# Performance work log

Measured on AMD Instinct MI355X. Metric: run time of the kernel, lower is better.

The kernel has to match this reference:

```python
import jax, jax.numpy as jnp
import numpy as np
import math

B, S, E, A = 8, 2048, 1024, 1024
NEG = -1e20

def setup_inputs() -> dict:
    key = jax.random.key(0)
    ks = jax.random.split(key, 6)
    scale = 1.0 / math.sqrt(E)
    return {
        "q": jax.random.normal(ks[0], (B, S, E), dtype=jnp.float32),
        "k": jax.random.normal(ks[1], (B, S, E), dtype=jnp.float32),
        "v": jax.random.normal(ks[2], (B, S, E), dtype=jnp.float32),
        "mask_pad": jnp.ones((B, S, S), dtype=jnp.int32),
        "Wq": jax.random.normal(ks[3], (E, A), dtype=jnp.float32) * scale,
        "Wk": jax.random.normal(ks[4], (E, A), dtype=jnp.float32) * scale,
        "Wv": jax.random.normal(ks[5], (E, A), dtype=jnp.float32) * scale,
    }

def reference(q, k, v, mask_pad, Wq, Wk, Wv):
    att_dim = Wq.shape[1]
    qp = jnp.einsum('bse,ea->bsa', q, Wq)
    kp = jnp.einsum('bse,ea->bsa', k, Wk)
    vp = jnp.einsum('bse,ea->bsa', v, Wv)
    # scores: [B, S, S]
    qk = jnp.einsum('bqa,bka->bqk', qp, kp) / jnp.sqrt(jnp.float32(att_dim))
    qk = jnp.where(mask_pad == 0, NEG, qk)
    # causal: torch.tril zeros out upper triangle, then zeros -> -1e20 (faithful quirk)
    seq = qk.shape[1]
    tril = jnp.tril(jnp.ones((seq, seq), dtype=bool))
    qk = jnp.where(tril[None, :, :], qk, 0.0)
    qk = jnp.where(qk == 0.0, NEG, qk)
    att_w = jax.nn.softmax(qk, axis=2)  # dropout p=0 -> identity
    return jnp.einsum('bqk,bka->bqa', att_w, vp)
```

## Files before the change

### kernel.cpp

```cpp
#include <hip/hip_runtime.h>
#include <math.h>

typedef __bf16 bf16x8 __attribute__((ext_vector_type(8)));
typedef float  f32x4  __attribute__((ext_vector_type(4)));
typedef unsigned short u16x8 __attribute__((ext_vector_type(8)));

#define NEGF (-1e20f)

__device__ __forceinline__ unsigned short f2bf(float f) {
  union { float f; unsigned u; } x; x.f = f;
  unsigned r = x.u + 0x7fffu + ((x.u >> 16) & 1u);
  return (unsigned short)(r >> 16);
}
__device__ __forceinline__ float bf2f(unsigned short h) {
  union { unsigned u; float f; } x; x.u = ((unsigned)h) << 16;
  return x.f;
}

__device__ __forceinline__ void gl16(const void* g, void* l) {
  __builtin_amdgcn_global_load_lds(
      (const __attribute__((address_space(1))) unsigned int*)g,
      (__attribute__((address_space(3))) unsigned int*)l, 16, 0, 0);
}
__device__ __forceinline__ unsigned lds_addr(const void* p) {
  return (unsigned)(unsigned long long)(const __attribute__((address_space(3))) char*)p;
}

#define DSR(dst, off) asm volatile("ds_read_b128 %0, %1" : "=v"(dst) : "v"(off))
#define LGKM0 asm volatile("s_waitcnt lgkmcnt(0)" ::: "memory")
#define VMC0  asm volatile("s_waitcnt vmcnt(0)" ::: "memory")
#define SBAR  __builtin_amdgcn_s_barrier()
#define SCH0  __builtin_amdgcn_sched_barrier(0)

__global__ __launch_bounds__(256) void k_cvt3(
    const float* __restrict__ q, const float* __restrict__ k, const float* __restrict__ v,
    unsigned short* __restrict__ qo, unsigned short* __restrict__ ko, unsigned short* __restrict__ vo) {
  const float* in = (blockIdx.y == 0) ? q : (blockIdx.y == 1) ? k : v;
  unsigned short* out = (blockIdx.y == 0) ? qo : (blockIdx.y == 1) ? ko : vo;
  size_t i = ((size_t)blockIdx.x * 256 + threadIdx.x) * 8;
  const float4* p = (const float4*)(in + i);
  float4 a = p[0], b = p[1];
  u16x8 o;
  o[0] = f2bf(a.x); o[1] = f2bf(a.y); o[2] = f2bf(a.z); o[3] = f2bf(a.w);
  o[4] = f2bf(b.x); o[5] = f2bf(b.y); o[6] = f2bf(b.z); o[7] = f2bf(b.w);
  *(u16x8*)(out + i) = o;
}

__global__ __launch_bounds__(256) void k_cvt_w(const float* __restrict__ W,
                                               unsigned short* __restrict__ WT) {
  __shared__ float t[32][33];
  const int tid = threadIdx.x;
  const int tx = tid & 31, ty = tid >> 5;
  const int e0 = blockIdx.y * 32, a0 = blockIdx.x * 32;
#pragma unroll
  for (int i = 0; i < 4; i++) {
    int el = ty + i * 8;
    t[el][tx] = W[(size_t)(e0 + el) * 1024 + a0 + tx];
  }
  __syncthreads();
#pragma unroll
  for (int i = 0; i < 4; i++) {
    int al = ty + i * 8;
    WT[(size_t)(a0 + al) * 1024 + e0 + tx] = f2bf(t[tx][al]);
  }
}

__global__ __launch_bounds__(256) void k_maskbits(const int* __restrict__ mask,
                                                  unsigned short* __restrict__ bits) {
  size_t t = (size_t)blockIdx.x * 256 + threadIdx.x;
  const int4* p = (const int4*)(mask + t * 16);
  int4 a = p[0], b = p[1], c = p[2], d = p[3];
  unsigned m = 0;
  m |= (a.x != 0) ? 1u : 0u;      m |= (a.y != 0) ? 2u : 0u;
  m |= (a.z != 0) ? 4u : 0u;      m |= (a.w != 0) ? 8u : 0u;
  m |= (b.x != 0) ? 16u : 0u;     m |= (b.y != 0) ? 32u : 0u;
  m |= (b.z != 0) ? 64u : 0u;     m |= (b.w != 0) ? 128u : 0u;
  m |= (c.x != 0) ? 256u : 0u;    m |= (c.y != 0) ? 512u : 0u;
  m |= (c.z != 0) ? 1024u : 0u;   m |= (c.w != 0) ? 2048u : 0u;
  m |= (d.x != 0) ? 4096u : 0u;   m |= (d.y != 0) ? 8192u : 0u;
  m |= (d.z != 0) ? 16384u : 0u;  m |= (d.w != 0) ? 32768u : 0u;
  bits[t] = (unsigned short)m;
}

__device__ __forceinline__ void tile128_gemm(
    const unsigned short* __restrict__ A, int lda,
    const unsigned short* __restrict__ Bt, int ldb,
    int brow, int bcol, int NT,
    unsigned short* AsBase, unsigned short* BsBase,
    int wr, int wc, int fr, int fq,
    f32x4 (&acc)[4][4])
{
  const int tid = threadIdx.x, wid = tid >> 6, l = tid & 63;
  const int sr = l >> 3;
  const int sc = ((l & 7) ^ sr) * 8;

  const unsigned short* ga = A + (size_t)(brow + wid * 32 + sr) * lda + sc;
  const unsigned short* gb = Bt + (size_t)(bcol + wid * 32 + sr) * ldb + sc;

  unsigned aA[4], aB[4];
#pragma unroll
  for (int m = 0; m < 4; m++) aA[m] = lds_addr(AsBase) + (unsigned)((wr * 64 + m * 16 + fr) * 128);
#pragma unroll
  for (int n = 0; n < 4; n++) aB[n] = lds_addr(BsBase) + (unsigned)((wc * 64 + n * 16 + fr) * 128);
  const unsigned ck0 = (unsigned)((fq ^ (fr & 7)) * 16);
  const unsigned ck1 = (unsigned)(((4 + fq) ^ (fr & 7)) * 16);

  auto stage = [&](int buf, int k0) {
    unsigned short* la = AsBase + buf * (128 * 64);
    unsigned short* lb = BsBase + buf * (128 * 64);
#pragma unroll
    for (int i = 0; i < 4; i++) {
      gl16(ga + (size_t)(8 * i) * lda + k0, la + (wid * 32 + 8 * i) * 64);
      gl16(gb + (size_t)(8 * i) * ldb + k0, lb + (wid * 32 + 8 * i) * 64);
    }
  };

  stage(0, 0);
  VMC0; SBAR;

  for (int t = 0; t < NT; ++t) {
    if (t + 1 < NT) stage((t + 1) & 1, (t + 1) << 6);
    const unsigned bo = (unsigned)((t & 1) * (128 * 64 * 2));
    u16x8 ar[4], br[4];
#pragma unroll
    for (int m = 0; m < 4; m++) DSR(ar[m], aA[m] + bo + ck0);
#pragma unroll
    for (int n = 0; n < 4; n++) DSR(br[n], aB[n] + bo + ck0);
    LGKM0; SCH0;
    __builtin_amdgcn_s_setprio(1);
#pragma unroll
    for (int m = 0; m < 4; m++)
#pragma unroll
      for (int n = 0; n < 4; n++)
        acc[m][n] = __builtin_amdgcn_mfma_f32_16x16x32_bf16(
            __builtin_bit_cast(bf16x8, ar[m]), __builtin_bit_cast(bf16x8, br[n]), acc[m][n], 0, 0, 0);
    __builtin_amdgcn_s_setprio(0);
    u16x8 ar2[4], br2[4];
#pragma unroll
    for (int m = 0; m < 4; m++) DSR(ar2[m], aA[m] + bo + ck1);
#pragma unroll
    for (int n = 0; n < 4; n++) DSR(br2[n], aB[n] + bo + ck1);
    LGKM0; SCH0;
    __builtin_amdgcn_s_setprio(1);
#pragma unroll
    for (int m = 0; m < 4; m++)
#pragma unroll
      for (int n = 0; n < 4; n++)
        acc[m][n] = __builtin_amdgcn_mfma_f32_16x16x32_bf16(
            __builtin_bit_cast(bf16x8, ar2[m]), __builtin_bit_cast(bf16x8, br2[n]), acc[m][n], 0, 0, 0);
    __builtin_amdgcn_s_setprio(0);
    SCH0;
    VMC0;
    SBAR;
  }
}

__global__ __launch_bounds__(512, 2) void k_proj256(
    const unsigned short* __restrict__ A, int lda,
    const unsigned short* __restrict__ Bt, int ldb,
    unsigned short* __restrict__ C, int ldc, int K, float scale)
{
  const int nwg = gridDim.x * gridDim.y;
  int lin = blockIdx.y * gridDim.x + blockIdx.x;
  int swz = (lin & 7) * (nwg >> 3) + (lin >> 3);
  const int bx = swz % gridDim.x, by = swz / gridDim.x;
  const int brow = by * 256, bcol = bx * 256;

  __shared__ unsigned short As[2][256 * 64];
  __shared__ unsigned short Bs[2][256 * 64];

  const int tid = threadIdx.x, w = tid >> 6, l = tid & 63;
  const int wr = w >> 2, wc = w & 3;
  const int fr = l & 15, fq = l >> 4;
  const int sr = l >> 3;
  const int sc = ((l & 7) ^ sr) * 8;

  const unsigned short* ga = A + (size_t)(brow + w * 32 + sr) * lda + sc;
  const unsigned short* gb = Bt + (size_t)(bcol + w * 32 + sr) * ldb + sc;

  f32x4 acc[8][4] = {};

  unsigned aA[8], aB[4];
#pragma unroll
  for (int m = 0; m < 8; m++) aA[m] = lds_addr(&As[0][0]) + (unsigned)((wr * 128 + m * 16 + fr) * 128);
#pragma unroll
  for (int n = 0; n < 4; n++) aB[n] = lds_addr(&Bs[0][0]) + (unsigned)((wc * 64 + n * 16 + fr) * 128);
  const unsigned ck0 = (unsigned)((fq ^ (fr & 7)) * 16);
  const unsigned ck1 = (unsigned)(((4 + fq) ^ (fr & 7)) * 16);

  auto stage = [&](int buf, int k0) {
#pragma unroll
    for (int i = 0; i < 4; i++) {
      gl16(ga + (size_t)(8 * i) * lda + k0, &As[buf][(w * 32 + 8 * i) * 64]);
      gl16(gb + (size_t)(8 * i) * ldb + k0, &Bs[buf][(w * 32 + 8 * i) * 64]);
    }
  };

  const int NT = K >> 6;
  stage(0, 0);
  VMC0; SBAR;
  for (int t = 0; t < NT; ++t) {
    if (t + 1 < NT) stage((t + 1) & 1, (t + 1) << 6);
    const unsigned bo = (unsigned)((t & 1) * (256 * 64 * 2));
    u16x8 ar[8], br[4];
#pragma unroll
    for (int m = 0; m < 8; m++) DSR(ar[m], aA[m] + bo + ck0);
#pragma unroll
    for (int n = 0; n < 4; n++) DSR(br[n], aB[n] + bo + ck0);
    LGKM0; SCH0;
    __builtin_amdgcn_s_setprio(1);
#pragma unroll
    for (int m = 0; m < 8; m++)
#pragma unroll
      for (int n = 0; n < 4; n++)
        acc[m][n] = __builtin_amdgcn_mfma_f32_16x16x32_bf16(
            __builtin_bit_cast(bf16x8, ar[m]), __builtin_bit_cast(bf16x8, br[n]), acc[m][n], 0, 0, 0);
    __builtin_amdgcn_s_setprio(0);
    u16x8 ar2[8], br2[4];
#pragma unroll
    for (int m = 0; m < 8; m++) DSR(ar2[m], aA[m] + bo + ck1);
#pragma unroll
    for (int n = 0; n < 4; n++) DSR(br2[n], aB[n] + bo + ck1);
    LGKM0; SCH0;
    __builtin_amdgcn_s_setprio(1);
#pragma unroll
    for (int m = 0; m < 8; m++)
#pragma unroll
      for (int n = 0; n < 4; n++)
        acc[m][n] = __builtin_amdgcn_mfma_f32_16x16x32_bf16(
            __builtin_bit_cast(bf16x8, ar2[m]), __builtin_bit_cast(bf16x8, br2[n]), acc[m][n], 0, 0, 0);
    __builtin_amdgcn_s_setprio(0);
    SCH0;
    VMC0; SBAR;
  }

#pragma unroll
  for (int m = 0; m < 8; m++)
#pragma unroll
    for (int n = 0; n < 4; n++)
#pragma unroll
      for (int r = 0; r < 4; r++) {
        int rg = brow + wr * 128 + m * 16 + fq * 4 + r;
        int cg = bcol + wc * 64 + n * 16 + fr;
        C[(size_t)rg * ldc + cg] = f2bf(acc[m][n][r] * scale);
      }
}

__global__ __launch_bounds__(256, 2) void k_scores(
    const unsigned short* __restrict__ QP,
    const unsigned short* __restrict__ KP,
    unsigned short* __restrict__ S,
    const unsigned short* __restrict__ maskbits)
{
  int bid0 = blockIdx.x;
  int bid = (bid0 & 7) * 136 + (bid0 >> 3);
  const int b = bid / 136;
  int t0 = bid - b * 136;
  int by = (int)((sqrtf((float)(8 * t0 + 1)) - 1.0f) * 0.5f);
  if ((by + 1) * (by + 2) / 2 <= t0) by++;
  else if (by * (by + 1) / 2 > t0) by--;
  const int bx = t0 - (by * (by + 1)) / 2;
  const int brow = by * 128, bcol = bx * 128;

  const unsigned short* A  = QP + (size_t)b * (2048 * 1024);
  const unsigned short* Bt = KP + (size_t)b * (2048 * 1024);

  __shared__ unsigned short As[2][128 * 64];
  __shared__ unsigned short Bs[2][128 * 64];

  const int tid = threadIdx.x, wid = tid >> 6, lane = tid & 63;
  const int wr = wid >> 1, wc = wid & 1;
  const int fr = lane & 15, fq = lane >> 4;

  const unsigned short* bits = maskbits + (size_t)b * 2048 * 128;
  unsigned mbits[2] = {0u, 0u};
#pragma unroll
  for (int m = 0; m < 4; m++)
#pragma unroll
    for (int r = 0; r < 4; r++) {
      int qq = brow + wr * 64 + m * 16 + fq * 4 + r;
      unsigned long long mw =
          *(const unsigned long long*)(bits + (size_t)qq * 128 + ((bcol + wc * 64) >> 4));
#pragma unroll
      for (int n = 0; n < 4; n++) {
        int jj = (m << 4) | (n << 2) | r;
        unsigned bit = (unsigned)((mw >> (n * 16 + fr)) & 1ull);
        mbits[jj >> 5] |= bit << (jj & 31);
      }
    }
  asm volatile("" ::: "memory");

  f32x4 acc[4][4] = {};
  tile128_gemm(A, 1024, Bt, 1024, brow, bcol, 16, &As[0][0], &Bs[0][0],
               wr, wc, fr, fq, acc);

  unsigned short* Cb = S + (size_t)b * 2048 * 2048;
#pragma unroll
  for (int m = 0; m < 4; m++)
#pragma unroll
    for (int n = 0; n < 4; n++)
#pragma unroll
      for (int r = 0; r < 4; r++) {
        int jj = (m << 4) | (n << 2) | r;
        int qq = brow + wr * 64 + m * 16 + fq * 4 + r;
        int kk = bcol + wc * 64 + n * 16 + fr;
        float s = acc[m][n][r];
        if (!((mbits[jj >> 5] >> (jj & 31)) & 1u)) s = NEGF;
        if (kk > qq) s = NEGF;
        else if (s == 0.0f) s = NEGF;
        Cb[(size_t)qq * 2048 + kk] = f2bf(s);
      }
}

__global__ __launch_bounds__(256, 2) void k_pv(
    const unsigned short* __restrict__ P,
    const unsigned short* __restrict__ VpT,
    float* __restrict__ Out)
{
  const int b = blockIdx.z;
  const int by = (int)(gridDim.y - 1 - blockIdx.y);
  const int bx = blockIdx.x;
  const int brow = by * 128, bcol = bx * 128;

  const unsigned short* A  = P + (size_t)b * 2048 * 2048;
  const unsigned short* Bt = VpT + (size_t)b * 2048;

  __shared__ unsigned short As[2][128 * 64];
  __shared__ unsigned short Bs[2][128 * 64];

  const int tid = threadIdx.x, wid = tid >> 6, lane = tid & 63;
  const int wr = wid >> 1, wc = wid & 1;
  const int fr = lane & 15, fq = lane >> 4;

  f32x4 acc[4][4] = {};
  const int NT = (brow + 128) >> 6;
  tile128_gemm(A, 2048, Bt, 16384, brow, bcol, NT, &As[0][0], &Bs[0][0],
               wr, wc, fr, fq, acc);

  float* C = Out + (size_t)b * 2048 * 1024;
#pragma unroll
  for (int m = 0; m < 4; m++)
#pragma unroll
    for (int n = 0; n < 4; n++)
#pragma unroll
      for (int r = 0; r < 4; r++) {
        int rg = brow + wr * 64 + m * 16 + fq * 4 + r;
        int cg = bcol + wc * 64 + n * 16 + fr;
        C[(size_t)rg * 1024 + cg] = acc[m][n][r];
      }
}

__global__ __launch_bounds__(256) void k_softmax_bf(unsigned short* __restrict__ S) {
  const int row = blockIdx.x;
  const int qq = row & 2047;
  const int L = ((qq >> 7) + 1) << 7;
  const int tid = threadIdx.x;
  unsigned short* p = S + (size_t)row * 2048;
  float val[8];
  float mx = -3.0e38f;
  int cnt = 0;
  for (int i = tid; i * 4 < L; i += 256) {
    ushort4 u = *(const ushort4*)(p + i * 4);
    float a = bf2f(u.x), bb = bf2f(u.y), c = bf2f(u.z), d = bf2f(u.w);
    val[cnt] = a; val[cnt + 1] = bb; val[cnt + 2] = c; val[cnt + 3] = d;
    mx = fmaxf(fmaxf(fmaxf(mx, a), bb), fmaxf(c, d));
    cnt += 4;
  }
#pragma unroll
  for (int o = 32; o; o >>= 1) mx = fmaxf(mx, __shfl_xor(mx, o));
  __shared__ float sred[8];
  if ((tid & 63) == 0) sred[tid >> 6] = mx;
  __syncthreads();
  mx = fmaxf(fmaxf(sred[0], sred[1]), fmaxf(sred[2], sred[3]));
  float sum = 0.f;
  for (int j = 0; j < cnt; j++) { val[j] = __expf(val[j] - mx); sum += val[j]; }
#pragma unroll
  for (int o = 32; o; o >>= 1) sum += __shfl_xor(sum, o);
  if ((tid & 63) == 0) sred[4 + (tid >> 6)] = sum;
  __syncthreads();
  sum = (sred[4] + sred[5]) + (sred[6] + sred[7]);
  const float inv = 1.0f / sum;
  int j = 0;
  for (int i = tid; i * 4 < L; i += 256) {
    ushort4 o;
    o.x = f2bf(val[j] * inv);     o.y = f2bf(val[j + 1] * inv);
    o.z = f2bf(val[j + 2] * inv); o.w = f2bf(val[j + 3] * inv);
    *(ushort4*)(p + i * 4) = o;
    j += 4;
  }
}

extern "C" void kernel_launch(void* const* d_in, const int* in_sizes, int n_in,
                              void* d_out, int out_size, void* d_ws, size_t ws_size,
                              hipStream_t stream) {
  const float* q   = (const float*)d_in[0];
  const float* k   = (const float*)d_in[1];
  const float* v   = (const float*)d_in[2];
  const int*   msk = (const int*)d_in[3];
  const float* Wq  = (const float*)d_in[4];
  const float* Wk  = (const float*)d_in[5];
  const float* Wv  = (const float*)d_in[6];
  float* out = (float*)d_out;

  char* ws = (char*)d_ws;
  unsigned short* WqT = (unsigned short*)(ws + 0);
  unsigned short* WkT = (unsigned short*)(ws + 2097152);
  unsigned short* WvT = (unsigned short*)(ws + 4194304);
  unsigned short* qp  = (unsigned short*)(ws + 6291456);
  unsigned short* kp  = (unsigned short*)(ws + 39845888);
  unsigned short* vpT = (unsigned short*)(ws + 73400320);
  unsigned short* qbf = (unsigned short*)(ws + 106954752);
  unsigned short* kbf = (unsigned short*)(ws + 140509184);
  unsigned short* vbf = (unsigned short*)(ws + 174063616);
  unsigned short* P = (unsigned short*)(ws + 106954752);
  unsigned short* mbitsbuf = (unsigned short*)(ws + 207618048);

  dim3 blk(256), blk5(512);
  k_cvt3<<<dim3(8192, 3), blk, 0, stream>>>(q, k, v, qbf, kbf, vbf);
  k_cvt_w<<<dim3(32, 32), blk, 0, stream>>>(Wq, WqT);
  k_cvt_w<<<dim3(32, 32), blk, 0, stream>>>(Wk, WkT);
  k_cvt_w<<<dim3(32, 32), blk, 0, stream>>>(Wv, WvT);
  k_maskbits<<<dim3(8192), blk, 0, stream>>>(msk, mbitsbuf);

  k_proj256<<<dim3(4, 64), blk5, 0, stream>>>(qbf, 1024, WqT, 1024, qp, 1024, 1024, 0.03125f);
  k_proj256<<<dim3(4, 64), blk5, 0, stream>>>(kbf, 1024, WkT, 1024, kp, 1024, 1024, 1.0f);
  k_proj256<<<dim3(64, 4), blk5, 0, stream>>>(WvT, 1024, vbf, 1024, vpT, 16384, 1024, 1.0f);

  k_scores<<<dim3(1088), blk, 0, stream>>>(qp, kp, P, mbitsbuf);

  k_softmax_bf<<<dim3(16384), blk, 0, stream>>>(P);

  k_pv<<<dim3(8, 16, 8), blk, 0, stream>>>(P, vpT, out);
  (void)in_sizes; (void)n_in; (void)out_size; (void)ws_size;
}
```

Baseline: 365.8 us.

## Fuse fp32-to-bf16 activation conversion into projection GEMM loads

The projection GEMM now reads fp32 q/k/v directly, converts them to bf16 in registers and writes them into swizzled LDS, which removes the separate conversion kernel and its bf16 round trip through global memory. The three weight-transpose launches are merged into a single 3D-grid launch, and the mask-packing kernel now processes four chunks per thread with a quarter of the blocks. In exchange the GEMM loads twice as many bytes per element for one operand through ordinary register loads instead of direct-to-LDS loads, adding VGPR pressure and a VALU conversion step inside the main loop.

New measurement: 378.5 us. +3.5%, slower.

```diff
diff --git a/kernel.cpp b/kernel.cpp
--- a/kernel.cpp
+++ b/kernel.cpp
@@ -11,6 +11,10 @@
   union { float f; unsigned u; } x; x.f = f;
   unsigned r = x.u + 0x7fffu + ((x.u >> 16) & 1u);
   return (unsigned short)(r >> 16);
+}
+__device__ __forceinline__ unsigned short f2bfh(float f) {
+  __bf16 h = (__bf16)f;
+  return __builtin_bit_cast(unsigned short, h);
 }
 __device__ __forceinline__ float bf2f(unsigned short h) {
   union { unsigned u; float f; } x; x.u = ((unsigned)h) << 16;
@@ -32,22 +36,11 @@
 #define SBAR  __builtin_amdgcn_s_barrier()
 #define SCH0  __builtin_amdgcn_sched_barrier(0)
 
-__global__ __launch_bounds__(256) void k_cvt3(
-    const float* __restrict__ q, const float* __restrict__ k, const float* __restrict__ v,
-    unsigned short* __restrict__ qo, unsigned short* __restrict__ ko, unsigned short* __restrict__ vo) {
-  const float* in = (blockIdx.y == 0) ? q : (blockIdx.y == 1) ? k : v;
-  unsigned short* out = (blockIdx.y == 0) ? qo : (blockIdx.y == 1) ? ko : vo;
-  size_t i = ((size_t)blockIdx.x * 256 + threadIdx.x) * 8;
-  const float4* p = (const float4*)(in + i);
-  float4 a = p[0], b = p[1];
-  u16x8 o;
-  o[0] = f2bf(a.x); o[1] = f2bf(a.y); o[2] = f2bf(a.z); o[3] = f2bf(a.w);
-  o[4] = f2bf(b.x); o[5] = f2bf(b.y); o[6] = f2bf(b.z); o[7] = f2bf(b.w);
-  *(u16x8*)(out + i) = o;
-}
-
-__global__ __launch_bounds__(256) void k_cvt_w(const float* __restrict__ W,
-                                               unsigned short* __restrict__ WT) {
+__global__ __launch_bounds__(256) void k_cvt_w3(
+    const float* __restrict__ Wq, const float* __restrict__ Wk, const float* __restrict__ Wv,
+    unsigned short* __restrict__ Tq, unsigned short* __restrict__ Tk, unsigned short* __restrict__ Tv) {
+  const float* W = (blockIdx.z == 0) ? Wq : (blockIdx.z == 1) ? Wk : Wv;
+  unsigned short* WT = (blockIdx.z == 0) ? Tq : (blockIdx.z == 1) ? Tk : Tv;
   __shared__ float t[32][33];
   const int tid = threadIdx.x;
   const int tx = tid & 31, ty = tid >> 5;
@@ -67,19 +60,148 @@
 
 __global__ __launch_bounds__(256) void k_maskbits(const int* __restrict__ mask,
                                                   unsigned short* __restrict__ bits) {
-  size_t t = (size_t)blockIdx.x * 256 + threadIdx.x;
-  const int4* p = (const int4*)(mask + t * 16);
-  int4 a = p[0], b = p[1], c = p[2], d = p[3];
-  unsigned m = 0;
-  m |= (a.x != 0) ? 1u : 0u;      m |= (a.y != 0) ? 2u : 0u;
-  m |= (a.z != 0) ? 4u : 0u;      m |= (a.w != 0) ? 8u : 0u;
-  m |= (b.x != 0) ? 16u : 0u;     m |= (b.y != 0) ? 32u : 0u;
-  m |= (b.z != 0) ? 64u : 0u;     m |= (b.w != 0) ? 128u : 0u;
-  m |= (c.x != 0) ? 256u : 0u;    m |= (c.y != 0) ? 512u : 0u;
-  m |= (c.z != 0) ? 1024u : 0u;   m |= (c.w != 0) ? 2048u : 0u;
-  m |= (d.x != 0) ? 4096u : 0u;   m |= (d.y != 0) ? 8192u : 0u;
-  m |= (d.z != 0) ? 16384u : 0u;  m |= (d.w != 0) ? 32768u : 0u;
-  bits[t] = (unsigned short)m;
+#pragma unroll
+  for (int it = 0; it < 4; it++) {
+    size_t t = (size_t)it * 524288 + (size_t)blockIdx.x * 256 + threadIdx.x;
+    const int4* p = (const int4*)(mask + t * 16);
+    int4 a = p[0], b = p[1], c = p[2], d = p[3];
+    unsigned m = 0;
+    m |= (a.x != 0) ? 1u : 0u;      m |= (a.y != 0) ? 2u : 0u;
+    m |= (a.z != 0) ? 4u : 0u;      m |= (a.w != 0) ? 8u : 0u;
+    m |= (b.x != 0) ? 16u : 0u;     m |= (b.y != 0) ? 32u : 0u;
+    m |= (b.z != 0) ? 64u : 0u;     m |= (b.w != 0) ? 128u : 0u;
+    m |= (c.x != 0) ? 256u : 0u;    m |= (c.y != 0) ? 512u : 0u;
+    m |= (c.z != 0) ? 1024u : 0u;   m |= (c.w != 0) ? 2048u : 0u;
+    m |= (d.x != 0) ? 4096u : 0u;   m |= (d.y != 0) ? 8192u : 0u;
+    m |= (d.z != 0) ? 16384u : 0u;  m |= (d.w != 0) ? 32768u : 0u;
+    bits[t] = (unsigned short)m;
+  }
+}
+
+template<int FSIDE>
+__global__ __launch_bounds__(512, 2) void k_proj256(
+    const float* __restrict__ F, int ldf,
+    const unsigned short* __restrict__ H, int ldh,
+    unsigned short* __restrict__ C, int ldc, float scale)
+{
+  const int nwg = gridDim.x * gridDim.y;
+  int lin = blockIdx.y * gridDim.x + blockIdx.x;
+  int swz = (lin & 7) * (nwg >> 3) + (lin >> 3);
+  const int bx = swz % gridDim.x, by = swz / gridDim.x;
+  const int brow = by * 256, bcol = bx * 256;
+
+  __shared__ unsigned short As[2][256 * 64];
+  __shared__ unsigned short Bs[2][256 * 64];
+
+  const int tid = threadIdx.x, w = tid >> 6, l = tid & 63;
+  const int wr = w >> 2, wc = w & 3;
+  const int fr = l & 15, fq = l >> 4;
+
+  const int sr4 = tid >> 3;
+  const int scn = tid & 7;
+  const int hr = l >> 3;
+  const int hc = ((l & 7) ^ hr) * 8;
+
+  const int fbase = (FSIDE == 0) ? brow : bcol;
+  const int hbase = (FSIDE == 0) ? bcol : brow;
+  const float* gF = F + (size_t)(fbase + sr4 * 4) * ldf + scn * 8;
+  const unsigned short* gH = H + (size_t)(hbase + w * 32 + hr) * ldh + hc;
+
+  unsigned short* Fl = (FSIDE == 0) ? &As[0][0] : &Bs[0][0];
+  unsigned short* Hl = (FSIDE == 0) ? &Bs[0][0] : &As[0][0];
+
+  f32x4 acc[8][4] = {};
+
+  unsigned aA[8], aB[4];
+#pragma unroll
+  for (int m = 0; m < 8; m++) aA[m] = lds_addr(&As[0][0]) + (unsigned)((wr * 128 + m * 16 + fr) * 128);
+#pragma unroll
+  for (int n = 0; n < 4; n++) aB[n] = lds_addr(&Bs[0][0]) + (unsigned)((wc * 64 + n * 16 + fr) * 128);
+  const unsigned ck0 = (unsigned)((fq ^ (fr & 7)) * 16);
+  const unsigned ck1 = (unsigned)(((4 + fq) ^ (fr & 7)) * 16);
+
+  float4 fa[8];
+  auto loadF = [&](int k0) {
+#pragma unroll
+    for (int i = 0; i < 4; i++) {
+      const float* p = gF + (size_t)i * ldf + k0;
+      fa[2 * i]     = *(const float4*)p;
+      fa[2 * i + 1] = *(const float4*)(p + 4);
+    }
+  };
+  auto writeF = [&](int buf) {
+    unsigned short* lb = Fl + buf * (256 * 64);
+#pragma unroll
+    for (int i = 0; i < 4; i++) {
+      int row = sr4 * 4 + i;
+      u16x8 o;
+      o[0] = f2bfh(fa[2 * i].x);     o[1] = f2bfh(fa[2 * i].y);
+      o[2] = f2bfh(fa[2 * i].z);     o[3] = f2bfh(fa[2 * i].w);
+      o[4] = f2bfh(fa[2 * i + 1].x); o[5] = f2bfh(fa[2 * i + 1].y);
+      o[6] = f2bfh(fa[2 * i + 1].z); o[7] = f2bfh(fa[2 * i + 1].w);
+      *(u16x8*)&lb[row * 64 + ((scn ^ (row & 7)) * 8)] = o;
+    }
+  };
+  auto stageH = [&](int buf, int k0) {
+    unsigned short* lb = Hl + buf * (256 * 64);
+#pragma unroll
+    for (int i = 0; i < 4; i++)
+      gl16(gH + (size_t)(8 * i) * ldh + k0, lb + (w * 32 + 8 * i) * 64);
+  };
+
+  const int NT = 16;
+  loadF(0); stageH(0, 0);
+  VMC0;
+  writeF(0);
+  LGKM0; SBAR;
+
+  for (int t = 0; t < NT; ++t) {
+    if (t + 1 < NT) { loadF((t + 1) << 6); stageH((t + 1) & 1, (t + 1) << 6); SCH0; }
+    const unsigned bo = (unsigned)((t & 1) * (256 * 64 * 2));
+    u16x8 ar[8], br[4];
+#pragma unroll
+    for (int m = 0; m < 8; m++) DSR(ar[m], aA[m] + bo + ck0);
+#pragma unroll
+    for (int n = 0; n < 4; n++) DSR(br[n], aB[n] + bo + ck0);
+    LGKM0; SCH0;
+    __builtin_amdgcn_s_setprio(1);
+#pragma unroll
+    for (int m = 0; m < 8; m++)
+#pragma unroll
+      for (int n = 0; n < 4; n++)
+        acc[m][n] = __builtin_amdgcn_mfma_f32_16x16x32_bf16(
+            __builtin_bit_cast(bf16x8, ar[m]), __builtin_bit_cast(bf16x8, br[n]), acc[m][n], 0, 0, 0);
+    __builtin_amdgcn_s_setprio(0);
+    u16x8 ar2[8], br2[4];
+#pragma unroll
+    for (int m = 0; m < 8; m++) DSR(ar2[m], aA[m] + bo + ck1);
+#pragma unroll
+    for (int n = 0; n < 4; n++) DSR(br2[n], aB[n] + bo + ck1);
+    LGKM0; SCH0;
+    __builtin_amdgcn_s_setprio(1);
+#pragma unroll
+    for (int m = 0; m < 8; m++)
+#pragma unroll
+      for (int n = 0; n < 4; n++)
+        acc[m][n] = __builtin_amdgcn_mfma_f32_16x16x32_bf16(
+            __builtin_bit_cast(bf16x8, ar2[m]), __builtin_bit_cast(bf16x8, br2[n]), acc[m][n], 0, 0, 0);
+    __builtin_amdgcn_s_setprio(0);
+    SCH0;
+    VMC0;
+    if (t + 1 < NT) writeF((t + 1) & 1);
+    LGKM0; SBAR;
+  }
+
+#pragma unroll
+  for (int m = 0; m < 8; m++)
+#pragma unroll
+    for (int n = 0; n < 4; n++)
+#pragma unroll
+      for (int r = 0; r < 4; r++) {
+        int rg = brow + wr * 128 + m * 16 + fq * 4 + r;
+        int cg = bcol + wc * 64 + n * 16 + fr;
+        C[(size_t)rg * ldc + cg] = f2bf(acc[m][n][r] * scale);
+      }
 }
 
 __device__ __forceinline__ void tile128_gemm(
@@ -153,97 +275,6 @@
     VMC0;
     SBAR;
   }
-}
-
-__global__ __launch_bounds__(512, 2) void k_proj256(
-    const unsigned short* __restrict__ A, int lda,
-    const unsigned short* __restrict__ Bt, int ldb,
-    unsigned short* __restrict__ C, int ldc, int K, float scale)
-{
-  const int nwg = gridDim.x * gridDim.y;
-  int lin = blockIdx.y * gridDim.x + blockIdx.x;
-  int swz = (lin & 7) * (nwg >> 3) + (lin >> 3);
-  const int bx = swz % gridDim.x, by = swz / gridDim.x;
-  const int brow = by * 256, bcol = bx * 256;
-
-  __shared__ unsigned short As[2][256 * 64];
-  __shared__ unsigned short Bs[2][256 * 64];
-
-  const int tid = threadIdx.x, w = tid >> 6, l = tid & 63;
-  const int wr = w >> 2, wc = w & 3;
-  const int fr = l & 15, fq = l >> 4;
-  const int sr = l >> 3;
-  const int sc = ((l & 7) ^ sr) * 8;
-
-  const unsigned short* ga = A + (size_t)(brow + w * 32 + sr) * lda + sc;
-  const unsigned short* gb = Bt + (size_t)(bcol + w * 32 + sr) * ldb + sc;
-
-  f32x4 acc[8][4] = {};
-
-  unsigned aA[8], aB[4];
-#pragma unroll
-  for (int m = 0; m < 8; m++) aA[m] = lds_addr(&As[0][0]) + (unsigned)((wr * 128 + m * 16 + fr) * 128);
-#pragma unroll
-  for (int n = 0; n < 4; n++) aB[n] = lds_addr(&Bs[0][0]) + (unsigned)((wc * 64 + n * 16 + fr) * 128);
-  const unsigned ck0 = (unsigned)((fq ^ (fr & 7)) * 16);
-  const unsigned ck1 = (unsigned)(((4 + fq) ^ (fr & 7)) * 16);
-
-  auto stage = [&](int buf, int k0) {
-#pragma unroll
-    for (int i = 0; i < 4; i++) {
-      gl16(ga + (size_t)(8 * i) * lda + k0, &As[buf][(w * 32 + 8 * i) * 64]);
-      gl16(gb + (size_t)(8 * i) * ldb + k0, &Bs[buf][(w * 32 + 8 * i) * 64]);
-    }
-  };
-
-  const int NT = K >> 6;
-  stage(0, 0);
-  VMC0; SBAR;
-  for (int t = 0; t < NT; ++t) {
-    if (t + 1 < NT) stage((t + 1) & 1, (t + 1) << 6);
-    const unsigned bo = (unsigned)((t & 1) * (256 * 64 * 2));
-    u16x8 ar[8], br[4];
-#pragma unroll
-    for (int m = 0; m < 8; m++) DSR(ar[m], aA[m] + bo + ck0);
-#pragma unroll
-    for (int n = 0; n < 4; n++) DSR(br[n], aB[n] + bo + ck0);
-    LGKM0; SCH0;
-    __builtin_amdgcn_s_setprio(1);
-#pragma unroll
-    for (int m = 0; m < 8; m++)
-#pragma unroll
-      for (int n = 0; n < 4; n++)
-        acc[m][n] = __builtin_amdgcn_mfma_f32_16x16x32_bf16(
-            __builtin_bit_cast(bf16x8, ar[m]), __builtin_bit_cast(bf16x8, br[n]), acc[m][n], 0, 0, 0);
-    __builtin_amdgcn_s_setprio(0);
-    u16x8 ar2[8], br2[4];
-#pragma unroll
-    for (int m = 0; m < 8; m++) DSR(ar2[m], aA[m] + bo + ck1);
-#pragma unroll
-    for (int n = 0; n < 4; n++) DSR(br2[n], aB[n] + bo + ck1);
-    LGKM0; SCH0;
-    __builtin_amdgcn_s_setprio(1);
-#pragma unroll
-    for (int m = 0; m < 8; m++)
-#pragma unroll
-      for (int n = 0; n < 4; n++)
-        acc[m][n] = __builtin_amdgcn_mfma_f32_16x16x32_bf16(
-            __builtin_bit_cast(bf16x8, ar2[m]), __builtin_bit_cast(bf16x8, br2[n]), acc[m][n], 0, 0, 0);
-    __builtin_amdgcn_s_setprio(0);
-    SCH0;
-    VMC0; SBAR;
-  }
-
-#pragma unroll
-  for (int m = 0; m < 8; m++)
-#pragma unroll
-    for (int n = 0; n < 4; n++)
-#pragma unroll
-      for (int r = 0; r < 4; r++) {
-        int rg = brow + wr * 128 + m * 16 + fq * 4 + r;
-        int cg = bcol + wc * 64 + n * 16 + fr;
-        C[(size_t)rg * ldc + cg] = f2bf(acc[m][n][r] * scale);
-      }
 }
 
 __global__ __launch_bounds__(256, 2) void k_scores(
@@ -409,22 +440,16 @@
   unsigned short* qp  = (unsigned short*)(ws + 6291456);
   unsigned short* kp  = (unsigned short*)(ws + 39845888);
   unsigned short* vpT = (unsigned short*)(ws + 73400320);
-  unsigned short* qbf = (unsigned short*)(ws + 106954752);
-  unsigned short* kbf = (unsigned short*)(ws + 140509184);
-  unsigned short* vbf = (unsigned short*)(ws + 174063616);
-  unsigned short* P = (unsigned short*)(ws + 106954752);
+  unsigned short* P   = (unsigned short*)(ws + 106954752);
   unsigned short* mbitsbuf = (unsigned short*)(ws + 207618048);
 
   dim3 blk(256), blk5(512);
-  k_cvt3<<<dim3(8192, 3), blk, 0, stream>>>(q, k, v, qbf, kbf, vbf);
-  k_cvt_w<<<dim3(32, 32), blk, 0, stream>>>(Wq, WqT);
-  k_cvt_w<<<dim3(32, 32), blk, 0, stream>>>(Wk, WkT);
-  k_cvt_w<<<dim3(32, 32), blk, 0, stream>>>(Wv, WvT);
-  k_maskbits<<<dim3(8192), blk, 0, stream>>>(msk, mbitsbuf);
-
-  k_proj256<<<dim3(4, 64), blk5, 0, stream>>>(qbf, 1024, WqT, 1024, qp, 1024, 1024, 0.03125f);
-  k_proj256<<<dim3(4, 64), blk5, 0, stream>>>(kbf, 1024, WkT, 1024, kp, 1024, 1024, 1.0f);
-  k_proj256<<<dim3(64, 4), blk5, 0, stream>>>(WvT, 1024, vbf, 1024, vpT, 16384, 1024, 1.0f);
+  k_cvt_w3<<<dim3(32, 32, 3), blk, 0, stream>>>(Wq, Wk, Wv, WqT, WkT, WvT);
+  k_maskbits<<<dim3(2048), blk, 0, stream>>>(msk, mbitsbuf);
+
+  k_proj256<0><<<dim3(4, 64), blk5, 0, stream>>>(q, 1024, WqT, 1024, qp, 1024, 0.03125f);
+  k_proj256<0><<<dim3(4, 64), blk5, 0, stream>>>(k, 1024, WkT, 1024, kp, 1024, 1.0f);
+  k_proj256<1><<<dim3(64, 4), blk5, 0, stream>>>(v, 1024, WvT, 1024, vpT, 16384, 1.0f);
 
   k_scores<<<dim3(1088), blk, 0, stream>>>(qp, kp, P, mbitsbuf);
 
```

## Enlarge scores and PV GEMM tiles to 256x256 with shared core

Applied to the files above, without the earlier changes.

Replaces the 128x128 tiled scores and PV kernels with 256x256 tiles on 512-thread blocks, reusing a common gemm256_core that is also used by the projection kernel. Causal block granularity becomes 256, so the softmax row length and skipped tiles are adjusted to match. Larger tiles raise data reuse per loaded byte but compute more masked work along the diagonal and reduce the number of blocks, which may hurt load balance. Also merges the three weight conversions into one launch and widens the input conversion to 16 elements per thread using native bf16 casts.

Result: slower. 433.8 us (+18.6%).

```diff
diff --git a/kernel.cpp b/kernel.cpp
--- a/kernel.cpp
+++ b/kernel.cpp
@@ -11,6 +11,10 @@
   union { float f; unsigned u; } x; x.f = f;
   unsigned r = x.u + 0x7fffu + ((x.u >> 16) & 1u);
   return (unsigned short)(r >> 16);
+}
+__device__ __forceinline__ unsigned short f2bfh(float f) {
+  __bf16 h = (__bf16)f;
+  return __builtin_bit_cast(unsigned short, h);
 }
 __device__ __forceinline__ float bf2f(unsigned short h) {
   union { unsigned u; float f; } x; x.u = ((unsigned)h) << 16;
@@ -37,17 +41,23 @@
     unsigned short* __restrict__ qo, unsigned short* __restrict__ ko, unsigned short* __restrict__ vo) {
   const float* in = (blockIdx.y == 0) ? q : (blockIdx.y == 1) ? k : v;
   unsigned short* out = (blockIdx.y == 0) ? qo : (blockIdx.y == 1) ? ko : vo;
-  size_t i = ((size_t)blockIdx.x * 256 + threadIdx.x) * 8;
+  size_t i = ((size_t)blockIdx.x * 256 + threadIdx.x) * 16;
   const float4* p = (const float4*)(in + i);
-  float4 a = p[0], b = p[1];
-  u16x8 o;
-  o[0] = f2bf(a.x); o[1] = f2bf(a.y); o[2] = f2bf(a.z); o[3] = f2bf(a.w);
-  o[4] = f2bf(b.x); o[5] = f2bf(b.y); o[6] = f2bf(b.z); o[7] = f2bf(b.w);
-  *(u16x8*)(out + i) = o;
-}
-
-__global__ __launch_bounds__(256) void k_cvt_w(const float* __restrict__ W,
-                                               unsigned short* __restrict__ WT) {
+  float4 a = p[0], b = p[1], c = p[2], d = p[3];
+  u16x8 o0, o1;
+  o0[0] = f2bfh(a.x); o0[1] = f2bfh(a.y); o0[2] = f2bfh(a.z); o0[3] = f2bfh(a.w);
+  o0[4] = f2bfh(b.x); o0[5] = f2bfh(b.y); o0[6] = f2bfh(b.z); o0[7] = f2bfh(b.w);
+  o1[0] = f2bfh(c.x); o1[1] = f2bfh(c.y); o1[2] = f2bfh(c.z); o1[3] = f2bfh(c.w);
+  o1[4] = f2bfh(d.x); o1[5] = f2bfh(d.y); o1[6] = f2bfh(d.z); o1[7] = f2bfh(d.w);
+  *(u16x8*)(out + i) = o0;
+  *(u16x8*)(out + i + 8) = o1;
+}
+
+__global__ __launch_bounds__(256) void k_cvt_w3(
+    const float* __restrict__ Wq, const float* __restrict__ Wk, const float* __restrict__ Wv,
+    unsigned short* __restrict__ Tq, unsigned short* __restrict__ Tk, unsigned short* __restrict__ Tv) {
+  const float* W = (blockIdx.z == 0) ? Wq : (blockIdx.z == 1) ? Wk : Wv;
+  unsigned short* WT = (blockIdx.z == 0) ? Tq : (blockIdx.z == 1) ? Tk : Tv;
   __shared__ float t[32][33];
   const int tid = threadIdx.x;
   const int tx = tid & 31, ty = tid >> 5;
@@ -82,83 +92,80 @@
   bits[t] = (unsigned short)m;
 }
 
-__device__ __forceinline__ void tile128_gemm(
+__device__ __forceinline__ void gemm256_core(
     const unsigned short* __restrict__ A, int lda,
     const unsigned short* __restrict__ Bt, int ldb,
     int brow, int bcol, int NT,
-    unsigned short* AsBase, unsigned short* BsBase,
-    int wr, int wc, int fr, int fq,
-    f32x4 (&acc)[4][4])
+    unsigned short* As0, unsigned short* Bs0,
+    f32x4 (&acc)[8][4])
 {
-  const int tid = threadIdx.x, wid = tid >> 6, l = tid & 63;
-  const int sr = l >> 3;
-  const int sc = ((l & 7) ^ sr) * 8;
-
-  const unsigned short* ga = A + (size_t)(brow + wid * 32 + sr) * lda + sc;
-  const unsigned short* gb = Bt + (size_t)(bcol + wid * 32 + sr) * ldb + sc;
-
-  unsigned aA[4], aB[4];
-#pragma unroll
-  for (int m = 0; m < 4; m++) aA[m] = lds_addr(AsBase) + (unsigned)((wr * 64 + m * 16 + fr) * 128);
-#pragma unroll
-  for (int n = 0; n < 4; n++) aB[n] = lds_addr(BsBase) + (unsigned)((wc * 64 + n * 16 + fr) * 128);
+  const int tid = threadIdx.x, w = tid >> 6, l = tid & 63;
+  const int wr = w >> 2, wc = w & 3;
+  const int fr = l & 15, fq = l >> 4;
+  const int hr = l >> 3;
+  const int hc = ((l & 7) ^ hr) * 8;
+
+  const unsigned short* ga = A + (size_t)(brow + w * 32 + hr) * lda + hc;
+  const unsigned short* gb = Bt + (size_t)(bcol + w * 32 + hr) * ldb + hc;
+
+  unsigned aA[8], aB[4];
+#pragma unroll
+  for (int m = 0; m < 8; m++) aA[m] = lds_addr(As0) + (unsigned)((wr * 128 + m * 16 + fr) * 128);
+#pragma unroll
+  for (int n = 0; n < 4; n++) aB[n] = lds_addr(Bs0) + (unsigned)((wc * 64 + n * 16 + fr) * 128);
   const unsigned ck0 = (unsigned)((fq ^ (fr & 7)) * 16);
   const unsigned ck1 = (unsigned)(((4 + fq) ^ (fr & 7)) * 16);
 
   auto stage = [&](int buf, int k0) {
-    unsigned short* la = AsBase + buf * (128 * 64);
-    unsigned short* lb = BsBase + buf * (128 * 64);
 #pragma unroll
     for (int i = 0; i < 4; i++) {
-      gl16(ga + (size_t)(8 * i) * lda + k0, la + (wid * 32 + 8 * i) * 64);
-      gl16(gb + (size_t)(8 * i) * ldb + k0, lb + (wid * 32 + 8 * i) * 64);
+      gl16(ga + (size_t)(8 * i) * lda + k0, As0 + buf * (256 * 64) + (w * 32 + 8 * i) * 64);
+      gl16(gb + (size_t)(8 * i) * ldb + k0, Bs0 + buf * (256 * 64) + (w * 32 + 8 * i) * 64);
     }
   };
 
   stage(0, 0);
   VMC0; SBAR;
-
   for (int t = 0; t < NT; ++t) {
     if (t + 1 < NT) stage((t + 1) & 1, (t + 1) << 6);
-    const unsigned bo = (unsigned)((t & 1) * (128 * 64 * 2));
-    u16x8 ar[4], br[4];
-#pragma unroll
-    for (int m = 0; m < 4; m++) DSR(ar[m], aA[m] + bo + ck0);
+    const unsigned bo = (unsigned)((t & 1) * (256 * 64 * 2));
+    u16x8 ar[8], br[4];
+#pragma unroll
+    for (int m = 0; m < 8; m++) DSR(ar[m], aA[m] + bo + ck0);
 #pragma unroll
     for (int n = 0; n < 4; n++) DSR(br[n], aB[n] + bo + ck0);
     LGKM0; SCH0;
     __builtin_amdgcn_s_setprio(1);
 #pragma unroll
-    for (int m = 0; m < 4; m++)
+    for (int m = 0; m < 8; m++)
 #pragma unroll
       for (int n = 0; n < 4; n++)
         acc[m][n] = __builtin_amdgcn_mfma_f32_16x16x32_bf16(
             __builtin_bit_cast(bf16x8, ar[m]), __builtin_bit_cast(bf16x8, br[n]), acc[m][n], 0, 0, 0);
     __builtin_amdgcn_s_setprio(0);
-    u16x8 ar2[4], br2[4];
-#pragma unroll
-    for (int m = 0; m < 4; m++) DSR(ar2[m], aA[m] + bo + ck1);
+    u16x8 ar2[8], br2[4];
+#pragma unroll
+    for (int m = 0; m < 8; m++) DSR(ar2[m], aA[m] + bo + ck1);
 #pragma unroll
     for (int n = 0; n < 4; n++) DSR(br2[n], aB[n] + bo + ck1);
     LGKM0; SCH0;
     __builtin_amdgcn_s_setprio(1);
 #pragma unroll
-    for (int m = 0; m < 4; m++)
+    for (int m = 0; m < 8; m++)
 #pragma unroll
       for (int n = 0; n < 4; n++)
         acc[m][n] = __builtin_amdgcn_mfma_f32_16x16x32_bf16(
             __builtin_bit_cast(bf16x8, ar2[m]), __builtin_bit_cast(bf16x8, br2[n]), acc[m][n], 0, 0, 0);
     __builtin_amdgcn_s_setprio(0);
     SCH0;
-    VMC0;
-    SBAR;
+    VMC0; SBAR;
   }
 }
 
 __global__ __launch_bounds__(512, 2) void k_proj256(
     const unsigned short* __restrict__ A, int lda,
     const unsigned short* __restrict__ Bt, int ldb,
-    unsigned short* __restrict__ C, int ldc, int K, float scale)
+    unsigned short* __restrict__ C, int ldc, float scale)
 {
   const int nwg = gridDim.x * gridDim.y;
   int lin = blockIdx.y * gridDim.x + blockIdx.x;
@@ -168,71 +175,12 @@
 
   __shared__ unsigned short As[2][256 * 64];
   __shared__ unsigned short Bs[2][256 * 64];
-
   const int tid = threadIdx.x, w = tid >> 6, l = tid & 63;
   const int wr = w >> 2, wc = w & 3;
   const int fr = l & 15, fq = l >> 4;
-  const int sr = l >> 3;
-  const int sc = ((l & 7) ^ sr) * 8;
-
-  const unsigned short* ga = A + (size_t)(brow + w * 32 + sr) * lda + sc;
-  const unsigned short* gb = Bt + (size_t)(bcol + w * 32 + sr) * ldb + sc;
 
   f32x4 acc[8][4] = {};
-
-  unsigned aA[8], aB[4];
-#pragma unroll
-  for (int m = 0; m < 8; m++) aA[m] = lds_addr(&As[0][0]) + (unsigned)((wr * 128 + m * 16 + fr) * 128);
-#pragma unroll
-  for (int n = 0; n < 4; n++) aB[n] = lds_addr(&Bs[0][0]) + (unsigned)((wc * 64 + n * 16 + fr) * 128);
-  const unsigned ck0 = (unsigned)((fq ^ (fr & 7)) * 16);
-  const unsigned ck1 = (unsigned)(((4 + fq) ^ (fr & 7)) * 16);
-
-  auto stage = [&](int buf, int k0) {
-#pragma unroll
-    for (int i = 0; i < 4; i++) {
-      gl16(ga + (size_t)(8 * i) * lda + k0, &As[buf][(w * 32 + 8 * i) * 64]);
-      gl16(gb + (size_t)(8 * i) * ldb + k0, &Bs[buf][(w * 32 + 8 * i) * 64]);
-    }
-  };
-
-  const int NT = K >> 6;
-  stage(0, 0);
-  VMC0; SBAR;
-  for (int t = 0; t < NT; ++t) {
-    if (t + 1 < NT) stage((t + 1) & 1, (t + 1) << 6);
-    const unsigned bo = (unsigned)((t & 1) * (256 * 64 * 2));
-    u16x8 ar[8], br[4];
-#pragma unroll
-    for (int m = 0; m < 8; m++) DSR(ar[m], aA[m] + bo + ck0);
-#pragma unroll
-    for (int n = 0; n < 4; n++) DSR(br[n], aB[n] + bo + ck0);
-    LGKM0; SCH0;
-    __builtin_amdgcn_s_setprio(1);
-#pragma unroll
-    for (int m = 0; m < 8; m++)
-#pragma unroll
-      for (int n = 0; n < 4; n++)
-        acc[m][n] = __builtin_amdgcn_mfma_f32_16x16x32_bf16(
-            __builtin_bit_cast(bf16x8, ar[m]), __builtin_bit_cast(bf16x8, br[n]), acc[m][n], 0, 0, 0);
-    __builtin_amdgcn_s_setprio(0);
-    u16x8 ar2[8], br2[4];
-#pragma unroll
-    for (int m = 0; m < 8; m++) DSR(ar2[m], aA[m] + bo + ck1);
-#pragma unroll
-    for (int n = 0; n < 4; n++) DSR(br2[n], aB[n] + bo + ck1);
-    LGKM0; SCH0;
-    __builtin_amdgcn_s_setprio(1);
-#pragma unroll
-    for (int m = 0; m < 8; m++)
-#pragma unroll
-      for (int n = 0; n < 4; n++)
-        acc[m][n] = __builtin_amdgcn_mfma_f32_16x16x32_bf16(
-            __builtin_bit_cast(bf16x8, ar2[m]), __builtin_bit_cast(bf16x8, br2[n]), acc[m][n], 0, 0, 0);
-    __builtin_amdgcn_s_setprio(0);
-    SCH0;
-    VMC0; SBAR;
-  }
+  gemm256_core(A, lda, Bt, ldb, brow, bcol, 16, &As[0][0], &Bs[0][0], acc);
 
 #pragma unroll
   for (int m = 0; m < 8; m++)
@@ -246,39 +194,37 @@
       }
 }
 
-__global__ __launch_bounds__(256, 2) void k_scores(
+__global__ __launch_bounds__(512, 2) void k_scores256(
     const unsigned short* __restrict__ QP,
     const unsigned short* __restrict__ KP,
     unsigned short* __restrict__ S,
     const unsigned short* __restrict__ maskbits)
 {
-  int bid0 = blockIdx.x;
-  int bid = (bid0 & 7) * 136 + (bid0 >> 3);
-  const int b = bid / 136;
-  int t0 = bid - b * 136;
+  int bid = ((int)blockIdx.x & 7) * 36 + ((int)blockIdx.x >> 3);
+  const int b = bid / 36;
+  int t0 = bid - b * 36;
   int by = (int)((sqrtf((float)(8 * t0 + 1)) - 1.0f) * 0.5f);
   if ((by + 1) * (by + 2) / 2 <= t0) by++;
   else if (by * (by + 1) / 2 > t0) by--;
   const int bx = t0 - (by * (by + 1)) / 2;
-  const int brow = by * 128, bcol = bx * 128;
+  const int brow = by * 256, bcol = bx * 256;
 
   const unsigned short* A  = QP + (size_t)b * (2048 * 1024);
   const unsigned short* Bt = KP + (size_t)b * (2048 * 1024);
 
-  __shared__ unsigned short As[2][128 * 64];
-  __shared__ unsigned short Bs[2][128 * 64];
-
-  const int tid = threadIdx.x, wid = tid >> 6, lane = tid & 63;
-  const int wr = wid >> 1, wc = wid & 1;
-  const int fr = lane & 15, fq = lane >> 4;
+  __shared__ unsigned short As[2][256 * 64];
+  __shared__ unsigned short Bs[2][256 * 64];
+  const int tid = threadIdx.x, w = tid >> 6, l = tid & 63;
+  const int wr = w >> 2, wc = w & 3;
+  const int fr = l & 15, fq = l >> 4;
 
   const unsigned short* bits = maskbits + (size_t)b * 2048 * 128;
-  unsigned mbits[2] = {0u, 0u};
-#pragma unroll
-  for (int m = 0; m < 4; m++)
+  unsigned mbits[4] = {0u, 0u, 0u, 0u};
+#pragma unroll
+  for (int m = 0; m < 8; m++)
 #pragma unroll
     for (int r = 0; r < 4; r++) {
-      int qq = brow + wr * 64 + m * 16 + fq * 4 + r;
+      int qq = brow + wr * 128 + m * 16 + fq * 4 + r;
       unsigned long long mw =
           *(const unsigned long long*)(bits + (size_t)qq * 128 + ((bcol + wc * 64) >> 4));
 #pragma unroll
@@ -290,19 +236,18 @@
     }
   asm volatile("" ::: "memory");
 
-  f32x4 acc[4][4] = {};
-  tile128_gemm(A, 1024, Bt, 1024, brow, bcol, 16, &As[0][0], &Bs[0][0],
-               wr, wc, fr, fq, acc);
+  f32x4 acc[8][4] = {};
+  gemm256_core(A, 1024, Bt, 1024, brow, bcol, 16, &As[0][0], &Bs[0][0], acc);
 
   unsigned short* Cb = S + (size_t)b * 2048 * 2048;
 #pragma unroll
-  for (int m = 0; m < 4; m++)
+  for (int m = 0; m < 8; m++)
 #pragma unroll
     for (int n = 0; n < 4; n++)
 #pragma unroll
       for (int r = 0; r < 4; r++) {
         int jj = (m << 4) | (n << 2) | r;
-        int qq = brow + wr * 64 + m * 16 + fq * 4 + r;
+        int qq = brow + wr * 128 + m * 16 + fq * 4 + r;
         int kk = bcol + wc * 64 + n * 16 + fr;
         float s = acc[m][n][r];
         if (!((mbits[jj >> 5] >> (jj & 31)) & 1u)) s = NEGF;
@@ -312,7 +257,7 @@
       }
 }
 
-__global__ __launch_bounds__(256, 2) void k_pv(
+__global__ __launch_bounds__(512, 2) void k_pv256(
     const unsigned short* __restrict__ P,
     const unsigned short* __restrict__ VpT,
     float* __restrict__ Out)
@@ -320,31 +265,29 @@
   const int b = blockIdx.z;
   const int by = (int)(gridDim.y - 1 - blockIdx.y);
   const int bx = blockIdx.x;
-  const int brow = by * 128, bcol = bx * 128;
+  const int brow = by * 256, bcol = bx * 256;
 
   const unsigned short* A  = P + (size_t)b * 2048 * 2048;
   const unsigned short* Bt = VpT + (size_t)b * 2048;
 
-  __shared__ unsigned short As[2][128 * 64];
-  __shared__ unsigned short Bs[2][128 * 64];
-
-  const int tid = threadIdx.x, wid = tid >> 6, lane = tid & 63;
-  const int wr = wid >> 1, wc = wid & 1;
-  const int fr = lane & 15, fq = lane >> 4;
-
-  f32x4 acc[4][4] = {};
-  const int NT = (brow + 128) >> 6;
-  tile128_gemm(A, 2048, Bt, 16384, brow, bcol, NT, &As[0][0], &Bs[0][0],
-               wr, wc, fr, fq, acc);
+  __shared__ unsigned short As[2][256 * 64];
+  __shared__ unsigned short Bs[2][256 * 64];
+  const int tid = threadIdx.x, w = tid >> 6, l = tid & 63;
+  const int wr = w >> 2, wc = w & 3;
+  const int fr = l & 15, fq = l >> 4;
+
+  f32x4 acc[8][4] = {};
+  const int NT = (brow + 256) >> 6;
+  gemm256_core(A, 2048, Bt, 16384, brow, bcol, NT, &As[0][0], &Bs[0][0], acc);
 
   float* C = Out + (size_t)b * 2048 * 1024;
 #pragma unroll
-  for (int m = 0; m < 4; m++)
+  for (int m = 0; m < 8; m++)
 #pragma unroll
     for (int n = 0; n < 4; n++)
 #pragma unroll
       for (int r = 0; r < 4; r++) {
-        int rg = brow + wr * 64 + m * 16 + fq * 4 + r;
+        int rg = brow + wr * 128 + m * 16 + fq * 4 + r;
         int cg = bcol + wc * 64 + n * 16 + fr;
         C[(size_t)rg * 1024 + cg] = acc[m][n][r];
       }
@@ -353,7 +296,7 @@
 __global__ __launch_bounds__(256) void k_softmax_bf(unsigned short* __restrict__ S) {
   const int row = blockIdx.x;
   const int qq = row & 2047;
-  const int L = ((qq >> 7) + 1) << 7;
+  const int L = ((qq >> 8) + 1) << 8;
   const int tid = threadIdx.x;
   unsigned short* p = S + (size_t)row * 2048;
   float val[8];
@@ -416,20 +359,18 @@
   unsigned short* mbitsbuf = (unsigned short*)(ws + 207618048);
 
   dim3 blk(256), blk5(512);
-  k_cvt3<<<dim3(8192, 3), blk, 0, stream>>>(q, k, v, qbf, kbf, vbf);
-  k_cvt_w<<<dim3(32, 32), blk, 0, stream>>>(Wq, WqT);
-  k_cvt_w<<<dim3(32, 32), blk, 0, stream>>>(Wk, WkT);
-  k_cvt_w<<<dim3(32, 32), blk, 0, stream>>>(Wv, WvT);
+  k_cvt3<<<dim3(4096, 3), blk, 0, stream>>>(q, k, v, qbf, kbf, vbf);
+  k_cvt_w3<<<dim3(32, 32, 3), blk, 0, stream>>>(Wq, Wk, Wv, WqT, WkT, WvT);
   k_maskbits<<<dim3(8192), blk, 0, stream>>>(msk, mbitsbuf);
 
-  k_proj256<<<dim3(4, 64), blk5, 0, stream>>>(qbf, 1024, WqT, 1024, qp, 1024, 1024, 0.03125f);
-  k_proj256<<<dim3(4, 64), blk5, 0, stream>>>(kbf, 1024, WkT, 1024, kp, 1024, 1024, 1.0f);
-  k_proj256<<<dim3(64, 4), blk5, 0, stream>>>(WvT, 1024, vbf, 1024, vpT, 16384, 1024, 1.0f);
-
-  k_scores<<<dim3(1088), blk, 0, stream>>>(qp, kp, P, mbitsbuf);
+  k_proj256<<<dim3(4, 64), blk5, 0, stream>>>(qbf, 1024, WqT, 1024, qp, 1024, 0.03125f);
+  k_proj256<<<dim3(4, 64), blk5, 0, stream>>>(kbf, 1024, WkT, 1024, kp, 1024, 1.0f);
+  k_proj256<<<dim3(64, 4), blk5, 0, stream>>>(WvT, 1024, vbf, 1024, vpT, 16384, 1.0f);
+
+  k_scores256<<<dim3(288), blk5, 0, stream>>>(qp, kp, P, mbitsbuf);
 
   k_softmax_bf<<<dim3(16384), blk, 0, stream>>>(P);
 
-  k_pv<<<dim3(8, 16, 8), blk, 0, stream>>>(P, vpT, out);
+  k_pv256<<<dim3(4, 8, 8), blk5, 0, stream>>>(P, vpT, out);
   (void)in_sizes; (void)n_in; (void)out_size; (void)ws_size;
 }
```
